# Optimization experiments

Measured on AMD Instinct MI355X. Metric: run time of the kernel, lower is better.

## Reference

```python
import jax, jax.numpy as jnp
import numpy as np

NUM_HEADS = 16


def setup_inputs() -> dict:
    key = jax.random.key(0)
    ks = jax.random.split(key, 7)
    B, S, H = 4, 1024, 1024
    s = 0.02
    return {
        "x": jax.random.normal(ks[0], (B, S, H), dtype=jnp.float32),
        "Wq": jax.random.normal(ks[1], (H, H), dtype=jnp.float32) * s,
        "bq": jax.random.normal(ks[2], (H,), dtype=jnp.float32) * s,
        "Wk": jax.random.normal(ks[3], (H, H), dtype=jnp.float32) * s,
        "bk": jax.random.normal(ks[4], (H,), dtype=jnp.float32) * s,
        "Wv": jax.random.normal(ks[5], (H, H), dtype=jnp.float32) * s,
        "bv": jax.random.normal(ks[6], (H,), dtype=jnp.float32) * s,
    }


def _split_heads(y, num_heads):
    # rearrange 'b s (h c) -> h b s c'
    b, s, hid = y.shape
    c = hid // num_heads
    return y.reshape(b, s, num_heads, c).transpose(2, 0, 1, 3)


def reference(x, Wq, bq, Wk, bk, Wv, bv):
    h = NUM_HEADS
    head_size = x.shape[-1] // h
    # torch Linear: y = x @ W.T + b
    q = _split_heads(x @ Wq.T + bq, h)  # [h,b,s,c]
    k = _split_heads(x @ Wk.T + bk, h)
    v = _split_heads(x @ Wv.T + bv, h)
    scores = jnp.einsum('hbfc,hbtc->hbft', q, k) / jnp.sqrt(
        jnp.asarray(head_size, x.dtype))
    patterns = jax.nn.softmax(scores, axis=-1)  # softmax over t
    # NOTE: faithful to source, contracts over f (query axis) per
    # einsum('hbft,hbfc->hbtc', patterns, value)
    av = jnp.einsum('hbft,hbfc->hbtc', patterns, v)  # [h,b,t,c]
    # rearrange 'h b s c -> b s (c h)'  (channel-major interleave)
    out = av.transpose(1, 2, 3, 0)  # [b,s,c,h]
    b, s, c, hh = out.shape
    return out.reshape(b, s, c * hh)
```

## Files before the change

kernel.cpp:

```cpp
#include <hip/hip_runtime.h>
#include <hip/hip_bf16.h>

typedef short bf16x8 __attribute__((ext_vector_type(8)));
typedef short bf16x4 __attribute__((ext_vector_type(4)));
typedef float f32x4 __attribute__((ext_vector_type(4)));
typedef unsigned short u16;

#define MFMA32(a, b, c) __builtin_amdgcn_mfma_f32_16x16x32_bf16(a, b, c, 0, 0, 0)

#if defined(__has_builtin)
#if __has_builtin(__builtin_amdgcn_mfma_f32_16x16x16bf16_1k)
#define HAVE_MFMA16 1
#define MFMA16(a, b, c) __builtin_amdgcn_mfma_f32_16x16x16bf16_1k(a, b, c, 0, 0, 0)
#endif
#endif
#ifndef HAVE_MFMA16
static __device__ inline f32x4 mfma16_asm(bf16x4 a, bf16x4 b, f32x4 c) {
    f32x4 d;
    asm volatile("v_mfma_f32_16x16x16_bf16 %0, %1, %2, %3\n\ts_nop 7\n\ts_nop 7"
                 : "=v"(d) : "v"(a), "v"(b), "v"(c));
    return d;
}
#define MFMA16(a, b, c) mfma16_asm(a, b, c)
#endif

__device__ inline float fexp2(float x) {
#if defined(__has_builtin) && __has_builtin(__builtin_amdgcn_exp2f)
    return __builtin_amdgcn_exp2f(x);
#else
    return exp2f(x);
#endif
}

__device__ inline u16 f2bf(float f) {
    unsigned u = __float_as_uint(f);
    unsigned r = (u + 0x7fffu + ((u >> 16) & 1u)) >> 16;
    return (u16)r;
}

__device__ inline float bf2f(u16 v) {
    return __uint_as_float(((unsigned)v) << 16);
}

__device__ inline void gload_lds16(const void* g, void* l) {
    __builtin_amdgcn_global_load_lds(
        (const __attribute__((address_space(1))) void*)g,
        (__attribute__((address_space(3))) void*)l, 16, 0, 0);
}

#define BARRIER() __builtin_amdgcn_s_barrier()
#define VMCNT0() asm volatile("s_waitcnt vmcnt(0)" ::: "memory")

__device__ inline int swz(int row, int colbyte) {
    return row * 128 + (colbyte ^ ((row & 7) << 4));
}

__device__ inline int swzV(int row, int colbyte) {
    return row * 256 + (colbyte ^ ((row & 15) << 4));
}

__device__ inline void stage16k128_512(const u16* __restrict__ g, int gstride,
                                       u16* lds, int tid) {
#pragma unroll
    for (int j = 0; j < 2; j++) {
        int o = (tid + j * 512) * 16;
        int row = o >> 7;
        int colb = (o & 127) ^ ((row & 7) << 4);
        gload_lds16(g + row * gstride + (colb >> 1), (char*)lds + o);
    }
}

__device__ inline void stage16k256_512(const u16* __restrict__ g, int gstride,
                                       u16* lds, int tid) {
#pragma unroll
    for (int j = 0; j < 2; j++) {
        int o = (tid + j * 512) * 16;
        int row = o >> 8;
        int colb = (o & 255) ^ ((row & 15) << 4);
        gload_lds16(g + row * gstride + (colb >> 1), (char*)lds + o);
    }
}

__device__ inline void stage16k_256(const u16* __restrict__ g, int gstride,
                                    u16* lds, int tid) {
#pragma unroll
    for (int j = 0; j < 4; j++) {
        int o = (tid + j * 256) * 16;
        int row = o >> 7;
        int colb = (o & 127) ^ ((row & 7) << 4);
        gload_lds16(g + row * gstride + (colb >> 1), (char*)lds + o);
    }
}

__device__ inline void stage8k_256(const u16* __restrict__ g, int gstride,
                                   u16* lds, int tid) {
#pragma unroll
    for (int j = 0; j < 2; j++) {
        int o = (tid + j * 256) * 16;
        int row = o >> 7;
        int colb = (o & 127) ^ ((row & 7) << 4);
        gload_lds16(g + row * gstride + (colb >> 1), (char*)lds + o);
    }
}

__global__ void k_convert_all(const float* __restrict__ x,
                              const float* __restrict__ w0, const float* __restrict__ w1,
                              const float* __restrict__ w2,
                              u16* __restrict__ xb, u16* __restrict__ wb) {
    const int bid = blockIdx.x;
    const float* s;
    u16* d;
    int i;
    if (bid < 4096) {
        s = x; d = xb;
        i = bid * 1024 + threadIdx.x * 4;
    } else {
        int wsec = (bid - 4096) >> 10;
        int boff = (bid - 4096) & 1023;
        s = (wsec == 0) ? w0 : ((wsec == 1) ? w1 : w2);
        d = wb + wsec * 1048576;
        i = boff * 1024 + threadIdx.x * 4;
    }
    float4 v = *reinterpret_cast<const float4*>(s + i);
    ushort4 o;
    o.x = f2bf(v.x); o.y = f2bf(v.y); o.z = f2bf(v.z); o.w = f2bf(v.w);
    *reinterpret_cast<ushort4*>(d + i) = o;
}

__global__ __launch_bounds__(256, 6) void k_proj(
    const u16* __restrict__ xb, const u16* __restrict__ wb,
    const float* __restrict__ bq, const float* __restrict__ bk, const float* __restrict__ bv,
    u16* __restrict__ outQ, u16* __restrict__ outK, u16* __restrict__ outVt)
{
    __shared__ __align__(16) u16 As[8192];
    __shared__ __align__(16) u16 Bs[4096];
    const int tid = threadIdx.x;
    const int lane = tid & 63;
    const int w = tid >> 6;
    const int bid = blockIdx.x;
    const int xcd = bid & 7, idx = bid >> 3;
    const int mg = xcd & 3, ng = xcd >> 2;
    const int m0 = (mg * 8 + (idx & 7)) * 128;
    const int nfull = ng * 24 + (idx >> 3);
    const int widx = nfull >> 4;
    const int n0 = (nfull & 15) * 64;
    const u16* W = wb + widx * 1024 * 1024;
    const float* bias = (widx == 0) ? bq : ((widx == 1) ? bk : bv);

    const int wm = (w >> 1) * 64, wn = (w & 1) * 32;
    const int lm = lane & 15, lg = lane >> 4;

    f32x4 zero = {0.f, 0.f, 0.f, 0.f};
    f32x4 acc[4][2];
#pragma unroll
    for (int m = 0; m < 4; m++)
#pragma unroll
        for (int n = 0; n < 2; n++) acc[m][n] = zero;

    for (int it = 0; it < 16; ++it) {
        stage16k_256(xb + m0 * 1024 + it * 64, 1024, As, tid);
        stage8k_256(W + n0 * 1024 + it * 64, 1024, Bs, tid);
        __syncthreads();
        const char* Ab = (const char*)As;
        const char* Bb = (const char*)Bs;
#pragma unroll
        for (int kk = 0; kk < 2; kk++) {
            bf16x8 a[4], b[2];
#pragma unroll
            for (int m = 0; m < 4; m++)
                a[m] = *(const bf16x8*)(Ab + swz(wm + m * 16 + lm, kk * 64 + lg * 16));
#pragma unroll
            for (int n = 0; n < 2; n++)
                b[n] = *(const bf16x8*)(Bb + swz(wn + n * 16 + lm, kk * 64 + lg * 16));
#pragma unroll
            for (int m = 0; m < 4; m++)
#pragma unroll
                for (int n = 0; n < 2; n++)
                    acc[m][n] = MFMA32(a[m], b[n], acc[m][n]);
        }
        __syncthreads();
    }

#pragma unroll
    for (int n = 0; n < 2; n++) {
        int col = n0 + wn + n * 16 + lm;
        float bz = bias[col];
        int h = col >> 6, c = col & 63;
#pragma unroll
        for (int m = 0; m < 4; m++) {
#pragma unroll
            for (int r = 0; r < 4; r++) {
                int row = m0 + wm + m * 16 + lg * 4 + r;
                float v = acc[m][n][r] + bz;
                int bb = row >> 10, s = row & 1023;
                int hb = h * 4 + bb;
                if (widx == 0) {
                    outQ[(hb * 1024 + s) * 64 + c] = f2bf(v * 0.18033688011112042f);
                } else if (widx == 1) {
                    outK[(hb * 1024 + s) * 64 + c] = f2bf(v);
                } else {
                    outVt[(hb * 64 + c) * 1024 + s] = f2bf(v);
                }
            }
        }
    }
}

__global__ __launch_bounds__(512, 2) void k_stats(
    const u16* __restrict__ Q, const u16* __restrict__ K, float* __restrict__ linv_out)
{
    __shared__ __align__(16) u16 sK[2][8192];
    const int bid = blockIdx.x;
    const int hb = (bid & 7) * 8 + ((bid >> 3) & 7);
    const int fb = (bid >> 6) * 256;
    const int tid = threadIdx.x, lane = tid & 63, w = tid >> 6;
    const int lm = lane & 15, lg = lane >> 4;
    const u16* Qh = Q + hb * 65536;
    const u16* Kh = K + hb * 65536;

    bf16x8 a[2][2];
#pragma unroll
    for (int fg = 0; fg < 2; fg++) {
        const u16* qp = &Qh[(fb + w * 32 + fg * 16 + lm) * 64 + lg * 8];
        a[fg][0] = *(const bf16x8*)qp;
        a[fg][1] = *(const bf16x8*)(qp + 32);
    }

    float lrun[2][4] = {{0.f, 0.f, 0.f, 0.f}, {0.f, 0.f, 0.f, 0.f}};

    stage16k128_512(Kh, 64, sK[0], tid);
    VMCNT0();
    BARRIER();

    int cur = 0;
    for (int it = 0; it < 8; ++it) {
        if (it < 7)
            stage16k128_512(Kh + (it + 1) * 8192, 64, sK[cur ^ 1], tid);
        const char* base = (const char*)sK[cur];
#pragma unroll
        for (int n = 0; n < 8; n++) {
            int r = n * 16 + lm;
            bf16x8 b0 = *(const bf16x8*)(base + swz(r, lg * 16));
            bf16x8 b1 = *(const bf16x8*)(base + swz(r, 64 + lg * 16));
#pragma unroll
            for (int fg = 0; fg < 2; fg++) {
                f32x4 z = {0.f, 0.f, 0.f, 0.f};
                z = MFMA32(a[fg][0], b0, z);
                z = MFMA32(a[fg][1], b1, z);
                lrun[fg][0] += fexp2(z[0]);
                lrun[fg][1] += fexp2(z[1]);
                lrun[fg][2] += fexp2(z[2]);
                lrun[fg][3] += fexp2(z[3]);
            }
        }
        if (it < 7) {
            VMCNT0();
            BARRIER();
        }
        cur ^= 1;
    }
#pragma unroll
    for (int fg = 0; fg < 2; fg++) {
#pragma unroll
        for (int r = 0; r < 4; r++) {
            float s = lrun[fg][r];
            s += __shfl_xor(s, 1);
            s += __shfl_xor(s, 2);
            s += __shfl_xor(s, 4);
            s += __shfl_xor(s, 8);
            if (lm == 0)
                linv_out[hb * 1024 + fb + w * 32 + fg * 16 + lg * 4 + r] = 1.0f / s;
        }
    }
}

__global__ __launch_bounds__(512, 2) void k_av(
    const u16* __restrict__ Q, const u16* __restrict__ K, const u16* __restrict__ Vt,
    const float* __restrict__ linv, u16* __restrict__ av_sb)
{
    __shared__ __align__(16) u16 sQ[2][8192];
    __shared__ __align__(16) u16 sV[2][8192];
    __shared__ __align__(16) float linv_lds[1024];
    const int bid = blockIdx.x;
    const int hb = (bid & 7) * 8 + ((bid >> 3) & 7);
    const int tb = (bid >> 6) * 256;
    const int tid = threadIdx.x, lane = tid & 63, w = tid >> 6;
    const int lm = lane & 15, lg = lane >> 4;
    const u16* Qh = Q + hb * 65536;
    const u16* Kh = K + hb * 65536;
    const u16* Vh = Vt + hb * 65536;
    const float* lh = linv + hb * 1024;

    bf16x8 bK[2][2];
#pragma unroll
    for (int tg = 0; tg < 2; tg++) {
        const u16* kp = &Kh[(tb + w * 32 + tg * 16 + lm) * 64 + lg * 8];
        bK[tg][0] = *(const bf16x8*)kp;
        bK[tg][1] = *(const bf16x8*)(kp + 32);
    }

    f32x4 zero = {0.f, 0.f, 0.f, 0.f};
    f32x4 accv[2][4];
#pragma unroll
    for (int tg = 0; tg < 2; tg++)
#pragma unroll
        for (int m = 0; m < 4; m++) accv[tg][m] = zero;

    stage16k128_512(Qh, 64, sQ[0], tid);
    stage16k256_512(Vh, 1024, sV[0], tid);
    *reinterpret_cast<float2*>(&linv_lds[tid * 2]) =
        *reinterpret_cast<const float2*>(&lh[tid * 2]);
    VMCNT0();
    __syncthreads();

    int cur = 0;
    for (int it = 0; it < 8; ++it) {
        if (it < 7) {
            int fn = (it + 1) * 128;
            stage16k128_512(Qh + fn * 64, 64, sQ[cur ^ 1], tid);
            stage16k256_512(Vh + fn, 1024, sV[cur ^ 1], tid);
        }
        const char* Qb = (const char*)sQ[cur];
        const char* Vb = (const char*)sV[cur];
        const int fc = it * 128;

        bf16x4 afrag[2][8];
#pragma unroll
        for (int mq = 0; mq < 8; mq++) {
            bf16x8 aq0 = *(const bf16x8*)(Qb + swz(mq * 16 + lm, lg * 16));
            bf16x8 aq1 = *(const bf16x8*)(Qb + swz(mq * 16 + lm, 64 + lg * 16));
            float4 lv = *reinterpret_cast<const float4*>(&linv_lds[fc + mq * 16 + lg * 4]);
#pragma unroll
            for (int tg = 0; tg < 2; tg++) {
                f32x4 z = {0.f, 0.f, 0.f, 0.f};
                z = MFMA32(aq0, bK[tg][0], z);
                z = MFMA32(aq1, bK[tg][1], z);
                union { __hip_bfloat162 h2[2]; bf16x4 v4; } u;
                u.h2[0] = __float22bfloat162_rn(
                    make_float2(fexp2(z[0]) * lv.x, fexp2(z[1]) * lv.y));
                u.h2[1] = __float22bfloat162_rn(
                    make_float2(fexp2(z[2]) * lv.z, fexp2(z[3]) * lv.w));
                afrag[tg][mq] = u.v4;
            }
        }
        __builtin_amdgcn_s_setprio(1);
#pragma unroll
        for (int m = 0; m < 4; m++) {
#pragma unroll
            for (int kc = 0; kc < 8; kc++) {
                bf16x4 bv = *(const bf16x4*)(Vb + swzV(m * 16 + lm, kc * 32 + lg * 8));
#pragma unroll
                for (int tg = 0; tg < 2; tg++)
                    accv[tg][m] = MFMA16(afrag[tg][kc], bv, accv[tg][m]);
            }
        }
        __builtin_amdgcn_s_setprio(0);
        if (it < 7) {
            VMCNT0();
            BARRIER();
        }
        cur ^= 1;
    }

    const int h = hb >> 2, bb = hb & 3;
#pragma unroll
    for (int tg = 0; tg < 2; tg++) {
#pragma unroll
        for (int m = 0; m < 4; m++) {
#pragma unroll
            for (int r = 0; r < 4; r++) {
                int t = tb + w * 32 + tg * 16 + lg * 4 + r;
                av_sb[((bb * 1024 + t) * 16 + h) * 64 + m * 16 + lm] = f2bf(accv[tg][m][r]);
            }
        }
    }
}

__global__ __launch_bounds__(256) void k_interleave(
    const u16* __restrict__ av_sb, float* __restrict__ out)
{
    const int bid = blockIdx.x;
    const int bb = bid >> 7, ts = (bid & 127) * 8;
    const int c = threadIdx.x & 63, tl = threadIdx.x >> 6;
#pragma unroll
    for (int p = 0; p < 2; p++) {
        int t = ts + p * 4 + tl;
        const u16* src = &av_sb[(bb * 1024 + t) * 1024];
        float4 w[4];
#pragma unroll
        for (int q = 0; q < 4; q++) {
#pragma unroll
            for (int j = 0; j < 4; j++) {
                int h = q * 4 + j;
                ((float*)&w[q])[j] = bf2f(src[h * 64 + c]);
            }
        }
        float4* dst = (float4*)&out[(bb * 1024 + t) * 1024 + c * 16];
        dst[0] = w[0]; dst[1] = w[1]; dst[2] = w[2]; dst[3] = w[3];
    }
}

extern "C" void kernel_launch(void* const* d_in, const int* in_sizes, int n_in,
                              void* d_out, int out_size, void* d_ws, size_t ws_size,
                              hipStream_t stream) {
    const float* x  = (const float*)d_in[0];
    const float* Wq = (const float*)d_in[1];
    const float* bq = (const float*)d_in[2];
    const float* Wk = (const float*)d_in[3];
    const float* bk = (const float*)d_in[4];
    const float* Wv = (const float*)d_in[5];
    const float* bv = (const float*)d_in[6];
    float* out = (float*)d_out;
    char* ws = (char*)d_ws;

    u16* xb = (u16*)ws;
    u16* wb = (u16*)(ws + (8u << 20));
    u16* Qb = (u16*)(ws + (14u << 20));
    u16* Kb = (u16*)(ws + (22u << 20));
    u16* Vt = (u16*)(ws + (30u << 20));
    float* linv = (float*)(ws + (38u << 20));
    u16* av_sb = (u16*)ws;

    k_convert_all<<<7168, 256, 0, stream>>>(x, Wq, Wk, Wv, xb, wb);
    k_proj<<<1536, 256, 0, stream>>>(xb, wb, bq, bk, bv, Qb, Kb, Vt);
    k_stats<<<256, 512, 0, stream>>>(Qb, Kb, linv);
    k_av<<<256, 512, 0, stream>>>(Qb, Kb, Vt, linv, av_sb);
    k_interleave<<<512, 256, 0, stream>>>(av_sb, out);
}
```

Baseline: 104.4 us.

## Retile projection GEMM to 256x256 with 4-stage pipeline; deepen attention prefetch

The projection GEMM moves from 128x64 tiles with single-buffered 64-wide K slices to 256x256 tiles per 512-thread block. It uses 32-wide K slices in a 4-slot LDS ring with partial vmcnt waits, which raises data reuse per block and overlaps global-to-LDS loads with MFMA work. The stats and AV kernels go from double buffering to a 4-slot ring with three tiles prefetched ahead. The cost is a much smaller projection grid (192 blocks), possible LDS bank conflicts from the unswizzled 64-byte row layout, and higher LDS use that limits occupancy.

```diff
diff --git a/kernel.cpp b/kernel.cpp
--- a/kernel.cpp
+++ b/kernel.cpp
@@ -49,7 +49,7 @@
 }
 
 #define BARRIER() __builtin_amdgcn_s_barrier()
-#define VMCNT0() asm volatile("s_waitcnt vmcnt(0)" ::: "memory")
+#define VMCNT(n) asm volatile("s_waitcnt vmcnt(" #n ")" ::: "memory")
 
 __device__ inline int swz(int row, int colbyte) {
     return row * 128 + (colbyte ^ ((row & 7) << 4));
@@ -57,6 +57,17 @@
 
 __device__ inline int swzV(int row, int colbyte) {
     return row * 256 + (colbyte ^ ((row & 15) << 4));
+}
+
+__device__ inline void stage32k(const u16* __restrict__ g, int gstride,
+                                u16* lds, int tid) {
+#pragma unroll
+    for (int j = 0; j < 2; j++) {
+        int o = (tid + j * 512) * 16;
+        int row = o >> 6;
+        int colk = (o & 63) >> 1;
+        gload_lds16(g + row * gstride + colk, (char*)lds + o);
+    }
 }
 
 __device__ inline void stage16k128_512(const u16* __restrict__ g, int gstride,
@@ -77,28 +88,6 @@
         int o = (tid + j * 512) * 16;
         int row = o >> 8;
         int colb = (o & 255) ^ ((row & 15) << 4);
-        gload_lds16(g + row * gstride + (colb >> 1), (char*)lds + o);
-    }
-}
-
-__device__ inline void stage16k_256(const u16* __restrict__ g, int gstride,
-                                    u16* lds, int tid) {
-#pragma unroll
-    for (int j = 0; j < 4; j++) {
-        int o = (tid + j * 256) * 16;
-        int row = o >> 7;
-        int colb = (o & 127) ^ ((row & 7) << 4);
-        gload_lds16(g + row * gstride + (colb >> 1), (char*)lds + o);
-    }
-}
-
-__device__ inline void stage8k_256(const u16* __restrict__ g, int gstride,
-                                   u16* lds, int tid) {
-#pragma unroll
-    for (int j = 0; j < 2; j++) {
-        int o = (tid + j * 256) * 16;
-        int row = o >> 7;
-        int colb = (o & 127) ^ ((row & 7) << 4);
         gload_lds16(g + row * gstride + (colb >> 1), (char*)lds + o);
     }
 }
@@ -127,70 +116,84 @@
     *reinterpret_cast<ushort4*>(d + i) = o;
 }
 
-__global__ __launch_bounds__(256, 6) void k_proj(
+__global__ __launch_bounds__(512, 2) void k_proj(
     const u16* __restrict__ xb, const u16* __restrict__ wb,
     const float* __restrict__ bq, const float* __restrict__ bk, const float* __restrict__ bv,
     u16* __restrict__ outQ, u16* __restrict__ outK, u16* __restrict__ outVt)
 {
-    __shared__ __align__(16) u16 As[8192];
-    __shared__ __align__(16) u16 Bs[4096];
+    __shared__ __align__(16) u16 As[4][8192];
+    __shared__ __align__(16) u16 Bs[4][8192];
     const int tid = threadIdx.x;
     const int lane = tid & 63;
     const int w = tid >> 6;
     const int bid = blockIdx.x;
     const int xcd = bid & 7, idx = bid >> 3;
     const int mg = xcd & 3, ng = xcd >> 2;
-    const int m0 = (mg * 8 + (idx & 7)) * 128;
-    const int nfull = ng * 24 + (idx >> 3);
-    const int widx = nfull >> 4;
-    const int n0 = (nfull & 15) * 64;
+    const int m0 = (mg * 4 + (idx & 3)) * 256;
+    const int nfull = ng * 6 + (idx >> 2);
+    const int widx = nfull >> 2;
+    const int n0 = (nfull & 3) * 256;
     const u16* W = wb + widx * 1024 * 1024;
     const float* bias = (widx == 0) ? bq : ((widx == 1) ? bk : bv);
 
-    const int wm = (w >> 1) * 64, wn = (w & 1) * 32;
+    const int wm2 = w >> 2, wn4 = w & 3;
     const int lm = lane & 15, lg = lane >> 4;
 
     f32x4 zero = {0.f, 0.f, 0.f, 0.f};
-    f32x4 acc[4][2];
-#pragma unroll
-    for (int m = 0; m < 4; m++)
-#pragma unroll
-        for (int n = 0; n < 2; n++) acc[m][n] = zero;
-
-    for (int it = 0; it < 16; ++it) {
-        stage16k_256(xb + m0 * 1024 + it * 64, 1024, As, tid);
-        stage8k_256(W + n0 * 1024 + it * 64, 1024, Bs, tid);
-        __syncthreads();
-        const char* Ab = (const char*)As;
-        const char* Bb = (const char*)Bs;
-#pragma unroll
-        for (int kk = 0; kk < 2; kk++) {
-            bf16x8 a[4], b[2];
-#pragma unroll
-            for (int m = 0; m < 4; m++)
-                a[m] = *(const bf16x8*)(Ab + swz(wm + m * 16 + lm, kk * 64 + lg * 16));
-#pragma unroll
-            for (int n = 0; n < 2; n++)
-                b[n] = *(const bf16x8*)(Bb + swz(wn + n * 16 + lm, kk * 64 + lg * 16));
-#pragma unroll
-            for (int m = 0; m < 4; m++)
-#pragma unroll
-                for (int n = 0; n < 2; n++)
-                    acc[m][n] = MFMA32(a[m], b[n], acc[m][n]);
-        }
-        __syncthreads();
-    }
-
-#pragma unroll
-    for (int n = 0; n < 2; n++) {
-        int col = n0 + wn + n * 16 + lm;
+    f32x4 acc[8][4];
+#pragma unroll
+    for (int m = 0; m < 8; m++)
+#pragma unroll
+        for (int n = 0; n < 4; n++) acc[m][n] = zero;
+
+    stage32k(xb + m0 * 1024, 1024, As[0], tid);
+    stage32k(W + n0 * 1024, 1024, Bs[0], tid);
+    stage32k(xb + m0 * 1024 + 32, 1024, As[1], tid);
+    stage32k(W + n0 * 1024 + 32, 1024, Bs[1], tid);
+    stage32k(xb + m0 * 1024 + 64, 1024, As[2], tid);
+    stage32k(W + n0 * 1024 + 64, 1024, Bs[2], tid);
+    VMCNT(8);
+    BARRIER();
+
+    for (int kt = 0; kt < 32; ++kt) {
+        const int slot = kt & 3;
+        if (kt + 3 < 32) {
+            const int kn = kt + 3;
+            stage32k(xb + m0 * 1024 + kn * 32, 1024, As[kn & 3], tid);
+            stage32k(W + n0 * 1024 + kn * 32, 1024, Bs[kn & 3], tid);
+        }
+        const u16* Ab = As[slot];
+        const u16* Bb = Bs[slot];
+        bf16x8 a[8], b[4];
+#pragma unroll
+        for (int m = 0; m < 8; m++)
+            a[m] = *(const bf16x8*)&Ab[(wm2 * 128 + m * 16 + lm) * 32 + lg * 8];
+#pragma unroll
+        for (int n = 0; n < 4; n++)
+            b[n] = *(const bf16x8*)&Bb[(wn4 * 64 + n * 16 + lm) * 32 + lg * 8];
+        __builtin_amdgcn_s_setprio(1);
+#pragma unroll
+        for (int m = 0; m < 8; m++)
+#pragma unroll
+            for (int n = 0; n < 4; n++)
+                acc[m][n] = MFMA32(a[m], b[n], acc[m][n]);
+        __builtin_amdgcn_s_setprio(0);
+        if (kt <= 28) VMCNT(8);
+        else if (kt == 29) VMCNT(4);
+        else if (kt == 30) VMCNT(0);
+        if (kt < 31) BARRIER();
+    }
+
+#pragma unroll
+    for (int n = 0; n < 4; n++) {
+        int col = n0 + wn4 * 64 + n * 16 + lm;
         float bz = bias[col];
         int h = col >> 6, c = col & 63;
 #pragma unroll
-        for (int m = 0; m < 4; m++) {
+        for (int m = 0; m < 8; m++) {
 #pragma unroll
             for (int r = 0; r < 4; r++) {
-                int row = m0 + wm + m * 16 + lg * 4 + r;
+                int row = m0 + wm2 * 128 + m * 16 + lg * 4 + r;
                 float v = acc[m][n][r] + bz;
                 int bb = row >> 10, s = row & 1023;
                 int hb = h * 4 + bb;
@@ -209,7 +212,7 @@
 __global__ __launch_bounds__(512, 2) void k_stats(
     const u16* __restrict__ Q, const u16* __restrict__ K, float* __restrict__ linv_out)
 {
-    __shared__ __align__(16) u16 sK[2][8192];
+    __shared__ __align__(16) u16 sK[4][8192];
     const int bid = blockIdx.x;
     const int hb = (bid & 7) * 8 + ((bid >> 3) & 7);
     const int fb = (bid >> 6) * 256;
@@ -229,14 +232,15 @@
     float lrun[2][4] = {{0.f, 0.f, 0.f, 0.f}, {0.f, 0.f, 0.f, 0.f}};
 
     stage16k128_512(Kh, 64, sK[0], tid);
-    VMCNT0();
+    stage16k128_512(Kh + 8192, 64, sK[1], tid);
+    stage16k128_512(Kh + 16384, 64, sK[2], tid);
+    VMCNT(4);
     BARRIER();
 
-    int cur = 0;
     for (int it = 0; it < 8; ++it) {
-        if (it < 7)
-            stage16k128_512(Kh + (it + 1) * 8192, 64, sK[cur ^ 1], tid);
-        const char* base = (const char*)sK[cur];
+        if (it + 3 < 8)
+            stage16k128_512(Kh + (it + 3) * 8192, 64, sK[(it + 3) & 3], tid);
+        const char* base = (const char*)sK[it & 3];
 #pragma unroll
         for (int n = 0; n < 8; n++) {
             int r = n * 16 + lm;
@@ -253,11 +257,10 @@
                 lrun[fg][3] += fexp2(z[3]);
             }
         }
-        if (it < 7) {
-            VMCNT0();
-            BARRIER();
-        }
-        cur ^= 1;
+        if (it <= 4) VMCNT(4);
+        else if (it == 5) VMCNT(2);
+        else if (it == 6) VMCNT(0);
+        if (it < 7) BARRIER();
     }
 #pragma unroll
     for (int fg = 0; fg < 2; fg++) {
@@ -278,8 +281,8 @@
     const u16* __restrict__ Q, const u16* __restrict__ K, const u16* __restrict__ Vt,
     const float* __restrict__ linv, u16* __restrict__ av_sb)
 {
-    __shared__ __align__(16) u16 sQ[2][8192];
-    __shared__ __align__(16) u16 sV[2][8192];
+    __shared__ __align__(16) u16 sQ[4][8192];
+    __shared__ __align__(16) u16 sV[4][8192];
     __shared__ __align__(16) float linv_lds[1024];
     const int bid = blockIdx.x;
     const int hb = (bid & 7) * 8 + ((bid >> 3) & 7);
@@ -308,20 +311,23 @@
 
     stage16k128_512(Qh, 64, sQ[0], tid);
     stage16k256_512(Vh, 1024, sV[0], tid);
+    stage16k128_512(Qh + 8192, 64, sQ[1], tid);
+    stage16k256_512(Vh + 128, 1024, sV[1], tid);
+    stage16k128_512(Qh + 16384, 64, sQ[2], tid);
+    stage16k256_512(Vh + 256, 1024, sV[2], tid);
     *reinterpret_cast<float2*>(&linv_lds[tid * 2]) =
         *reinterpret_cast<const float2*>(&lh[tid * 2]);
-    VMCNT0();
+    VMCNT(8);
     __syncthreads();
 
-    int cur = 0;
     for (int it = 0; it < 8; ++it) {
-        if (it < 7) {
-            int fn = (it + 1) * 128;
-            stage16k128_512(Qh + fn * 64, 64, sQ[cur ^ 1], tid);
-            stage16k256_512(Vh + fn, 1024, sV[cur ^ 1], tid);
-        }
-        const char* Qb = (const char*)sQ[cur];
-        const char* Vb = (const char*)sV[cur];
+        if (it + 3 < 8) {
+            const int fn = (it + 3) * 128;
+            stage16k128_512(Qh + fn * 64, 64, sQ[(it + 3) & 3], tid);
+            stage16k256_512(Vh + fn, 1024, sV[(it + 3) & 3], tid);
+        }
+        const char* Qb = (const char*)sQ[it & 3];
+        const char* Vb = (const char*)sV[it & 3];
         const int fc = it * 128;
 
         bf16x4 afrag[2][8];
@@ -355,11 +361,10 @@
             }
         }
         __builtin_amdgcn_s_setprio(0);
-        if (it < 7) {
-            VMCNT0();
-            BARRIER();
-        }
-        cur ^= 1;
+        if (it <= 4) VMCNT(8);
+        else if (it == 5) VMCNT(4);
+        else if (it == 6) VMCNT(0);
+        if (it < 7) BARRIER();
     }
 
     const int h = hb >> 2, bb = hb & 3;
@@ -422,7 +427,7 @@
     u16* av_sb = (u16*)ws;
 
     k_convert_all<<<7168, 256, 0, stream>>>(x, Wq, Wk, Wv, xb, wb);
-    k_proj<<<1536, 256, 0, stream>>>(xb, wb, bq, bk, bv, Qb, Kb, Vt);
+    k_proj<<<192, 512, 0, stream>>>(xb, wb, bq, bk, bv, Qb, Kb, Vt);
     k_stats<<<256, 512, 0, stream>>>(Qb, Kb, linv);
     k_av<<<256, 512, 0, stream>>>(Qb, Kb, Vt, linv, av_sb);
     k_interleave<<<512, 256, 0, stream>>>(av_sb, out);
```

Result: slower. 130.7 us (+25.2%).

## Deepen LDS prefetch pipeline to four stages in stats and AV kernels

Applied to the files above, without the earlier changes.

Replaces the double-buffered K staging in k_stats, and the Q/V staging in k_av, with a four-slot ring buffer that prefetches three tiles ahead. Each iteration now waits only for its own tile using a partial vmcnt count instead of draining all outstanding loads, so global-to-LDS latency can overlap more compute. The cost is twice the shared memory. For k_av that comes to about 132 KB per block, which likely no longer allows the two blocks per CU the launch bounds request, so occupancy may drop.

```diff
diff --git a/kernel.cpp b/kernel.cpp
--- a/kernel.cpp
+++ b/kernel.cpp
@@ -49,7 +49,7 @@
 }
 
 #define BARRIER() __builtin_amdgcn_s_barrier()
-#define VMCNT0() asm volatile("s_waitcnt vmcnt(0)" ::: "memory")
+#define VMCNT(n) asm volatile("s_waitcnt vmcnt(" #n ")" ::: "memory")
 
 __device__ inline int swz(int row, int colbyte) {
     return row * 128 + (colbyte ^ ((row & 7) << 4));
@@ -57,6 +57,28 @@
 
 __device__ inline int swzV(int row, int colbyte) {
     return row * 256 + (colbyte ^ ((row & 15) << 4));
+}
+
+__device__ inline void stage16k_256(const u16* __restrict__ g, int gstride,
+                                    u16* lds, int tid) {
+#pragma unroll
+    for (int j = 0; j < 4; j++) {
+        int o = (tid + j * 256) * 16;
+        int row = o >> 7;
+        int colb = (o & 127) ^ ((row & 7) << 4);
+        gload_lds16(g + row * gstride + (colb >> 1), (char*)lds + o);
+    }
+}
+
+__device__ inline void stage8k_256(const u16* __restrict__ g, int gstride,
+                                   u16* lds, int tid) {
+#pragma unroll
+    for (int j = 0; j < 2; j++) {
+        int o = (tid + j * 256) * 16;
+        int row = o >> 7;
+        int colb = (o & 127) ^ ((row & 7) << 4);
+        gload_lds16(g + row * gstride + (colb >> 1), (char*)lds + o);
+    }
 }
 
 __device__ inline void stage16k128_512(const u16* __restrict__ g, int gstride,
@@ -77,28 +99,6 @@
         int o = (tid + j * 512) * 16;
         int row = o >> 8;
         int colb = (o & 255) ^ ((row & 15) << 4);
-        gload_lds16(g + row * gstride + (colb >> 1), (char*)lds + o);
-    }
-}
-
-__device__ inline void stage16k_256(const u16* __restrict__ g, int gstride,
-                                    u16* lds, int tid) {
-#pragma unroll
-    for (int j = 0; j < 4; j++) {
-        int o = (tid + j * 256) * 16;
-        int row = o >> 7;
-        int colb = (o & 127) ^ ((row & 7) << 4);
-        gload_lds16(g + row * gstride + (colb >> 1), (char*)lds + o);
-    }
-}
-
-__device__ inline void stage8k_256(const u16* __restrict__ g, int gstride,
-                                   u16* lds, int tid) {
-#pragma unroll
-    for (int j = 0; j < 2; j++) {
-        int o = (tid + j * 256) * 16;
-        int row = o >> 7;
-        int colb = (o & 127) ^ ((row & 7) << 4);
         gload_lds16(g + row * gstride + (colb >> 1), (char*)lds + o);
     }
 }
@@ -209,7 +209,7 @@
 __global__ __launch_bounds__(512, 2) void k_stats(
     const u16* __restrict__ Q, const u16* __restrict__ K, float* __restrict__ linv_out)
 {
-    __shared__ __align__(16) u16 sK[2][8192];
+    __shared__ __align__(16) u16 sK[4][8192];
     const int bid = blockIdx.x;
     const int hb = (bid & 7) * 8 + ((bid >> 3) & 7);
     const int fb = (bid >> 6) * 256;
@@ -229,14 +229,15 @@
     float lrun[2][4] = {{0.f, 0.f, 0.f, 0.f}, {0.f, 0.f, 0.f, 0.f}};
 
     stage16k128_512(Kh, 64, sK[0], tid);
-    VMCNT0();
+    stage16k128_512(Kh + 8192, 64, sK[1], tid);
+    stage16k128_512(Kh + 16384, 64, sK[2], tid);
+    VMCNT(4);
     BARRIER();
 
-    int cur = 0;
     for (int it = 0; it < 8; ++it) {
-        if (it < 7)
-            stage16k128_512(Kh + (it + 1) * 8192, 64, sK[cur ^ 1], tid);
-        const char* base = (const char*)sK[cur];
+        if (it + 3 < 8)
+            stage16k128_512(Kh + (it + 3) * 8192, 64, sK[(it + 3) & 3], tid);
+        const char* base = (const char*)sK[it & 3];
 #pragma unroll
         for (int n = 0; n < 8; n++) {
             int r = n * 16 + lm;
@@ -253,11 +254,10 @@
                 lrun[fg][3] += fexp2(z[3]);
             }
         }
-        if (it < 7) {
-            VMCNT0();
-            BARRIER();
-        }
-        cur ^= 1;
+        if (it <= 4) VMCNT(4);
+        else if (it == 5) VMCNT(2);
+        else if (it == 6) VMCNT(0);
+        if (it < 7) BARRIER();
     }
 #pragma unroll
     for (int fg = 0; fg < 2; fg++) {
@@ -278,8 +278,8 @@
     const u16* __restrict__ Q, const u16* __restrict__ K, const u16* __restrict__ Vt,
     const float* __restrict__ linv, u16* __restrict__ av_sb)
 {
-    __shared__ __align__(16) u16 sQ[2][8192];
-    __shared__ __align__(16) u16 sV[2][8192];
+    __shared__ __align__(16) u16 sQ[4][8192];
+    __shared__ __align__(16) u16 sV[4][8192];
     __shared__ __align__(16) float linv_lds[1024];
     const int bid = blockIdx.x;
     const int hb = (bid & 7) * 8 + ((bid >> 3) & 7);
@@ -308,20 +308,23 @@
 
     stage16k128_512(Qh, 64, sQ[0], tid);
     stage16k256_512(Vh, 1024, sV[0], tid);
+    stage16k128_512(Qh + 8192, 64, sQ[1], tid);
+    stage16k256_512(Vh + 128, 1024, sV[1], tid);
+    stage16k128_512(Qh + 16384, 64, sQ[2], tid);
+    stage16k256_512(Vh + 256, 1024, sV[2], tid);
     *reinterpret_cast<float2*>(&linv_lds[tid * 2]) =
         *reinterpret_cast<const float2*>(&lh[tid * 2]);
-    VMCNT0();
+    VMCNT(8);
     __syncthreads();
 
-    int cur = 0;
     for (int it = 0; it < 8; ++it) {
-        if (it < 7) {
-            int fn = (it + 1) * 128;
-            stage16k128_512(Qh + fn * 64, 64, sQ[cur ^ 1], tid);
-            stage16k256_512(Vh + fn, 1024, sV[cur ^ 1], tid);
-        }
-        const char* Qb = (const char*)sQ[cur];
-        const char* Vb = (const char*)sV[cur];
+        if (it + 3 < 8) {
+            const int fn = (it + 3) * 128;
+            stage16k128_512(Qh + fn * 64, 64, sQ[(it + 3) & 3], tid);
+            stage16k256_512(Vh + fn, 1024, sV[(it + 3) & 3], tid);
+        }
+        const char* Qb = (const char*)sQ[it & 3];
+        const char* Vb = (const char*)sV[it & 3];
         const int fc = it * 128;
 
         bf16x4 afrag[2][8];
@@ -355,11 +358,10 @@
             }
         }
         __builtin_amdgcn_s_setprio(0);
-        if (it < 7) {
-            VMCNT0();
-            BARRIER();
-        }
-        cur ^= 1;
+        if (it <= 4) VMCNT(8);
+        else if (it == 5) VMCNT(4);
+        else if (it == 6) VMCNT(0);
+        if (it < 7) BARRIER();
     }
 
     const int h = hb >> 2, bb = hb & 3;
```

Result: no change. 105.9 us (+1.4%).
